# Performance work log

Hardware: AMD Instinct MI355X
Metric: run time of the kernel (lower is better)

## Reference

```python
import jax, jax.numpy as jnp
import numpy as np

B, C, H, W = 16, 256, 96, 96
PLANES = 64            # inplanes * ratio = 256 * 0.25
HEADS = 4
EPS = 1e-5             # BatchNorm eps


def setup_inputs() -> dict:
    key = jax.random.key(0)
    ks = jax.random.split(key, 8)
    HW = H * W
    G = HW // HEADS    # group size of the grouped 1x1 conv over spatial-positions-as-channels
    return {
        "x": jax.random.normal(ks[0], (B, C, H, W), jnp.float32),
        # input_conv: Conv1x1(C->PLANES) -> BN -> ReLU -> Conv1x1(PLANES->C)
        "w1": jax.random.normal(ks[1], (PLANES, C), jnp.float32) * (1.0 / np.sqrt(C)),
        "b1": jax.random.normal(ks[2], (PLANES,), jnp.float32) * 0.01,
        "gamma": jnp.ones((PLANES,), jnp.float32),
        "beta": jnp.zeros((PLANES,), jnp.float32),
        "mean": jnp.zeros((PLANES,), jnp.float32),
        "var": jnp.ones((PLANES,), jnp.float32),
        "w2": jax.random.normal(ks[3], (C, PLANES), jnp.float32) * (1.0 / np.sqrt(PLANES)),
        "b2": jax.random.normal(ks[4], (C,), jnp.float32) * 0.01,
        # conv_mask: Conv2d(HW, HEADS, k=1, groups=HEADS) -> weight [HEADS, G], bias [HEADS]
        "wm": jax.random.normal(ks[5], (HEADS, G), jnp.float32) * (1.0 / np.sqrt(G)),
        "bm": jax.random.normal(ks[6], (HEADS,), jnp.float32) * 0.01,
    }


def reference(x, w1, b1, gamma, beta, mean, var, w2, b2, wm, bm):
    Bx, Cx, Hx, Wx = x.shape
    G = (Hx * Wx) // HEADS
    # ---- input_conv: 1x1 conv -> BN (inference) -> ReLU -> 1x1 conv ----
    h = jnp.einsum('bchw,pc->bphw', x, w1) + b1[None, :, None, None]
    scale = (gamma / jnp.sqrt(var + EPS))[None, :, None, None]
    h = jax.nn.relu((h - mean[None, :, None, None]) * scale + beta[None, :, None, None])
    y = jnp.einsum('bphw,cp->bchw', h, w2) + b2[None, :, None, None]
    # ---- treat spatial positions as channels: [B, HEADS, G, C] ----
    ix = y.transpose(0, 2, 3, 1).reshape(Bx, HEADS, G, Cx)
    # grouped 1x1 conv over HW-channels -> logits [B, HEADS, C]
    logits = jnp.einsum('bhgc,hg->bhc', ix, wm) + bm[None, :, None]
    # softmax over channel axis (torch dim=2 of [B, HEADS, C, 1])
    mask = jax.nn.softmax(logits, axis=2)
    # context pooling matmul: [B,HEADS,G,C] @ [B,HEADS,C,1] -> [B,HEADS,G]
    ctx = jnp.einsum('bhgc,bhc->bhg', ix, mask)
    context = ctx.reshape(Bx, 1, Hx, Wx)
    # fusion_types = ('channel_add',)
    return x + context
```

## Files before the change

### kernel.cpp

```cpp
#include <hip/hip_runtime.h>

#define Bn 16
#define Cn 256
#define HWn 9216
#define Pn 64
#define HEADSn 4
#define Gn 2304
#define STILE 64
#define TILES_PER_B (HWn / STILE)
#define NTILE (Bn * TILES_PER_B)
#define CHUNK 9
#define NBLK (NTILE / CHUNK)

typedef float f32x4 __attribute__((ext_vector_type(4)));
typedef short short4v __attribute__((ext_vector_type(4)));
typedef short short8 __attribute__((ext_vector_type(8)));

static __device__ __forceinline__ unsigned short f2bf(float f) {
    unsigned int b = __builtin_bit_cast(unsigned int, f);
    unsigned int r = b + 0x7FFFu + ((b >> 16) & 1u);
    return (unsigned short)(r >> 16);
}
static __device__ __forceinline__ float bf2f(unsigned short u) {
    unsigned int b = ((unsigned int)u) << 16;
    return __builtin_bit_cast(float, b);
}
static __device__ __forceinline__ void gload_lds16(const void* g, void* l) {
    __builtin_amdgcn_global_load_lds((const __attribute__((address_space(1))) void*)g,
                                     (__attribute__((address_space(3))) void*)l, 16, 0, 0);
}

__global__ __launch_bounds__(256)
void k0_prep(const float* __restrict__ w1, const float* __restrict__ b1,
             const float* __restrict__ gamma, const float* __restrict__ beta,
             const float* __restrict__ mean, const float* __restrict__ var,
             float* __restrict__ bcv, short* __restrict__ w1b)
{
    const int gid = blockIdx.x * 256 + threadIdx.x;
    if (gid < 2048) {
        const int row = gid >> 5;
        const float s = gamma[row] * rsqrtf(var[row] + 1e-5f);
        const float* p = w1 + gid * 8;
        short8 v;
        #pragma unroll
        for (int j = 0; j < 8; ++j) v[j] = (short)f2bf(p[j] * s);
        *reinterpret_cast<short8*>(&w1b[gid * 8]) = v;
    }
    if (gid < Pn) {
        const float s = gamma[gid] * rsqrtf(var[gid] + 1e-5f);
        bcv[gid] = (b1[gid] - mean[gid]) * s + beta[gid];
    }
}

__global__ __launch_bounds__(256, 1)
void k1_gemm(const float* __restrict__ x, const short* __restrict__ w1b,
             const float* __restrict__ bcv, const float* __restrict__ wm,
             float* __restrict__ hmp, short* __restrict__ hg)
{
    __shared__ float xl[2][Cn * STILE];
    __shared__ float hml[4][Pn];

    const int pid  = blockIdx.x;
    const int b    = pid >> 4;
    const int t0b  = (pid & 15) * CHUNK;
    const int t    = threadIdx.x;
    const int lane = t & 63;
    const int wv   = t >> 6;
    const int wvu  = __builtin_amdgcn_readfirstlane(wv);
    const int g    = lane >> 4;
    const int m16  = lane & 15;
    const int sbase = wv * 16 + m16;

    short8 af[4][8];
    #pragma unroll
    for (int rt = 0; rt < 4; ++rt)
        #pragma unroll
        for (int ks = 0; ks < 8; ++ks)
            af[rt][ks] = *reinterpret_cast<const short8*>(
                w1b + (rt * 16 + m16) * Cn + ks * 32 + g * 8);

    float bc[4][4];
    #pragma unroll
    for (int rt = 0; rt < 4; ++rt)
        #pragma unroll
        for (int r = 0; r < 4; ++r) bc[rt][r] = bcv[rt * 16 + g * 4 + r];

    float hmacc[4][4];
    #pragma unroll
    for (int rt = 0; rt < 4; ++rt)
        #pragma unroll
        for (int r = 0; r < 4; ++r) hmacc[rt][r] = 0.f;

    const float* xbb = x + (size_t)b * Cn * HWn;

    #define STAGE(buf, tile)                                                     \
        do {                                                                     \
            const int _s0 = (tile) * STILE;                                      \
            _Pragma("unroll")                                                    \
            for (int i = 0; i < 16; ++i) {                                       \
                const int cbase = wvu * 64 + i * 4;                              \
                const int c     = cbase + g;                                     \
                const int gc    = (c >> 3) & 3;                                  \
                const int soff  = (m16 * 4) ^ (gc << 4);                         \
                gload_lds16(xbb + (size_t)c * HWn + _s0 + soff,                  \
                            &xl[buf][cbase * 64]);                               \
            }                                                                    \
        } while (0)

    STAGE(0, t0b);
    __syncthreads();

    int cur = 0;
    for (int it = 0; it < CHUNK; ++it) {
        if (it + 1 < CHUNK) STAGE(cur ^ 1, t0b + it + 1);

        const int s0 = (t0b + it) * STILE;
        const float* xc = xl[cur];
        const int srd = sbase ^ (g << 4);

        f32x4 acc[4] = { {0,0,0,0}, {0,0,0,0}, {0,0,0,0}, {0,0,0,0} };
        #pragma unroll
        for (int ks = 0; ks < 8; ++ks) {
            short8 bf;
            #pragma unroll
            for (int j = 0; j < 8; ++j) {
                const int k = ks * 32 + g * 8 + j;
                bf[j] = (short)f2bf(xc[k * 64 + srd]);
            }
            #pragma unroll
            for (int rt = 0; rt < 4; ++rt)
                acc[rt] = __builtin_amdgcn_mfma_f32_16x16x32_bf16(af[rt][ks], bf, acc[rt], 0, 0, 0);
        }

        const float wmv = wm[s0 + sbase];
        short* hrow = hg + ((size_t)b * HWn + s0 + sbase) * Pn;
        #pragma unroll
        for (int rt = 0; rt < 4; ++rt) {
            short4v hv;
            #pragma unroll
            for (int r = 0; r < 4; ++r) {
                float h = acc[rt][r] + bc[rt][r];
                h = h > 0.f ? h : 0.f;
                hmacc[rt][r] = fmaf(h, wmv, hmacc[rt][r]);
                hv[r] = (short)f2bf(h);
            }
            *reinterpret_cast<short4v*>(hrow + rt * 16 + g * 4) = hv;
        }

        __syncthreads();
        cur ^= 1;
    }

    #pragma unroll
    for (int rt = 0; rt < 4; ++rt)
        #pragma unroll
        for (int r = 0; r < 4; ++r) {
            float v = hmacc[rt][r];
            v += __shfl_xor(v, 1); v += __shfl_xor(v, 2);
            v += __shfl_xor(v, 4); v += __shfl_xor(v, 8);
            hmacc[rt][r] = v;
        }
    if (m16 == 0) {
        #pragma unroll
        for (int rt = 0; rt < 4; ++rt) {
            f32x4 hv = { hmacc[rt][0], hmacc[rt][1], hmacc[rt][2], hmacc[rt][3] };
            *reinterpret_cast<f32x4*>(&hml[wv][rt * 16 + g * 4]) = hv;
        }
    }
    __syncthreads();
    if (t < Pn) hmp[pid * Pn + t] = hml[0][t] + hml[1][t] + hml[2][t] + hml[3][t];
}

__global__ __launch_bounds__(256)
void k2_mask(const float* __restrict__ hmp, const float* __restrict__ w2,
             const float* __restrict__ b2, const float* __restrict__ wm,
             float* __restrict__ wmix, float* __restrict__ bmix)
{
    __shared__ float hms[Pn];
    __shared__ float masks[Cn];
    __shared__ float red[4];
    __shared__ float part[4][Pn];

    const int bh = blockIdx.x;
    const int head = bh & (HEADSn - 1);
    const int t = threadIdx.x;
    const int l = t & 63;
    const int wv = t >> 6;

    {
        const int p = t & 63, q = t >> 6;
        part[q][p] = hmp[(bh * 4 + q) * Pn + p];
    }
    __syncthreads();
    if (t < Pn) hms[t] = part[0][t] + part[1][t] + part[2][t] + part[3][t];
    __syncthreads();

    float wsum = 0.f;
    for (int i = t; i < Gn; i += 256) wsum += wm[head * Gn + i];
    #pragma unroll
    for (int d = 1; d < 64; d <<= 1) wsum += __shfl_xor(wsum, d);
    if (l == 0) red[wv] = wsum;
    __syncthreads();
    wsum = red[0] + red[1] + red[2] + red[3];

    float lg = 0.f;
    #pragma unroll
    for (int k = 0; k < Pn; ++k) lg = fmaf(w2[t * Pn + k], hms[k], lg);
    lg = fmaf(b2[t], wsum, lg);

    float mx = lg;
    #pragma unroll
    for (int d = 1; d < 64; d <<= 1) mx = fmaxf(mx, __shfl_xor(mx, d));
    __syncthreads();
    if (l == 0) red[wv] = mx;
    __syncthreads();
    mx = fmaxf(fmaxf(red[0], red[1]), fmaxf(red[2], red[3]));
    const float ev = __expf(lg - mx);
    float sm = ev;
    #pragma unroll
    for (int d = 1; d < 64; d <<= 1) sm += __shfl_xor(sm, d);
    __syncthreads();
    if (l == 0) red[wv] = sm;
    __syncthreads();
    sm = red[0] + red[1] + red[2] + red[3];
    masks[t] = ev / sm;
    __syncthreads();

    {
        const int k = t & (Pn - 1);
        const int q = t >> 6;
        float wp = 0.f;
        #pragma unroll
        for (int i = 0; i < 64; ++i) {
            const int c = q * 64 + i;
            wp = fmaf(masks[c], w2[c * Pn + k], wp);
        }
        part[q][k] = wp;
    }
    __syncthreads();
    if (t < Pn) wmix[bh * Pn + t] = part[0][t] + part[1][t] + part[2][t] + part[3][t];

    float bp = masks[t] * b2[t];
    #pragma unroll
    for (int d = 1; d < 64; d <<= 1) bp += __shfl_xor(bp, d);
    __syncthreads();
    if (l == 0) red[wv] = bp;
    __syncthreads();
    if (t == 0) bmix[bh] = red[0] + red[1] + red[2] + red[3];
}

__global__ __launch_bounds__(256)
void k3_stream(const float* __restrict__ x, const short* __restrict__ hg,
               const float* __restrict__ wmix, const float* __restrict__ bmix,
               float* __restrict__ out)
{
    __shared__ float ctxl[STILE];

    const int bid  = blockIdx.x;
    const int b    = bid / TILES_PER_B;
    const int tile = bid % TILES_PER_B;
    const int s0   = tile * STILE;
    const int head = s0 / Gn;
    const int bh   = b * HEADSn + head;
    const int t    = threadIdx.x;

    if (t < STILE) {
        const short* hr = hg + ((size_t)b * HWn + s0 + t) * Pn;
        const float* wmx = wmix + bh * Pn;
        float acc = 0.f;
        #pragma unroll
        for (int i = 0; i < 8; ++i) {
            const short8 v = *reinterpret_cast<const short8*>(hr + i * 8);
            const f32x4 w0 = *reinterpret_cast<const f32x4*>(wmx + i * 8);
            const f32x4 w1v = *reinterpret_cast<const f32x4*>(wmx + i * 8 + 4);
            #pragma unroll
            for (int j = 0; j < 4; ++j) {
                acc = fmaf(bf2f((unsigned short)v[j]), w0[j], acc);
                acc = fmaf(bf2f((unsigned short)v[4 + j]), w1v[j], acc);
            }
        }
        ctxl[t] = acc + bmix[bh];
    }
    __syncthreads();

    const int c0 = t >> 4;
    const int s4 = t & 15;
    const f32x4 cv = *reinterpret_cast<const f32x4*>(&ctxl[s4 * 4]);
    const float* xb = x + (size_t)b * Cn * HWn + s0 + s4 * 4;
    float* ob = out + (size_t)b * Cn * HWn + s0 + s4 * 4;
    #pragma unroll
    for (int i = 0; i < 16; ++i) {
        const size_t off = (size_t)(c0 + 16 * i) * HWn;
        *reinterpret_cast<f32x4*>(ob + off) =
            *reinterpret_cast<const f32x4*>(xb + off) + cv;
    }
}

extern "C" void kernel_launch(void* const* d_in, const int* in_sizes, int n_in,
                              void* d_out, int out_size, void* d_ws, size_t ws_size,
                              hipStream_t stream)
{
    (void)in_sizes; (void)n_in; (void)out_size; (void)ws_size;
    const float* x     = (const float*)d_in[0];
    const float* w1    = (const float*)d_in[1];
    const float* b1    = (const float*)d_in[2];
    const float* gamma = (const float*)d_in[3];
    const float* beta  = (const float*)d_in[4];
    const float* mean  = (const float*)d_in[5];
    const float* var   = (const float*)d_in[6];
    const float* w2    = (const float*)d_in[7];
    const float* b2    = (const float*)d_in[8];
    const float* wm    = (const float*)d_in[9];

    float* out  = (float*)d_out;
    float* wsf  = (float*)d_ws;
    float* hmp  = wsf;
    float* wmix = hmp + NBLK * Pn;
    float* bmix = wmix + Bn * HEADSn * Pn;
    float* bcv  = bmix + 64;
    short* w1b  = (short*)(bcv + 64);
    short* hg   = w1b + Pn * Cn;

    k0_prep<<<dim3(8), dim3(256), 0, stream>>>(w1, b1, gamma, beta, mean, var, bcv, w1b);
    k1_gemm<<<dim3(NBLK), dim3(256), 0, stream>>>(x, w1b, bcv, wm, hmp, hg);
    k2_mask<<<dim3(Bn * HEADSn), dim3(256), 0, stream>>>(hmp, w2, b2, wm, wmix, bmix);
    k3_stream<<<dim3(NTILE), dim3(256), 0, stream>>>(x, hg, wmix, bmix, out);
}
```

Baseline: 107.8 us.

## Split k1 GEMM into many small single-tile blocks with bf16 LDS staging

Replaces the persistent k1 kernel (256 blocks, each looping over 9 double-buffered 64-column tiles via global_load_lds) with 4608 small 128-thread blocks that each handle one 32-column tile. x is loaded with plain vector loads, converted to bf16 with v_cvt_pk_bf16_f32 and stored to a swizzled LDS layout, so LDS traffic and per-element conversions in the MFMA loop are reduced. Per-block hm partials go straight to global memory and k2 now sums 18 partials per head. This trades software pipelining for occupancy-based latency hiding, and adds more partial-sum traffic plus block launch overhead.

```diff
diff --git a/kernel.cpp b/kernel.cpp
--- a/kernel.cpp
+++ b/kernel.cpp
@@ -9,12 +9,13 @@
 #define STILE 64
 #define TILES_PER_B (HWn / STILE)
 #define NTILE (Bn * TILES_PER_B)
-#define CHUNK 9
-#define NBLK (NTILE / CHUNK)
+#define T32_PER_B 288
+#define NBLK1 (Bn * T32_PER_B)
 
 typedef float f32x4 __attribute__((ext_vector_type(4)));
 typedef short short4v __attribute__((ext_vector_type(4)));
 typedef short short8 __attribute__((ext_vector_type(8)));
+typedef unsigned int uint2v __attribute__((ext_vector_type(2)));
 
 static __device__ __forceinline__ unsigned short f2bf(float f) {
     unsigned int b = __builtin_bit_cast(unsigned int, f);
@@ -25,9 +26,10 @@
     unsigned int b = ((unsigned int)u) << 16;
     return __builtin_bit_cast(float, b);
 }
-static __device__ __forceinline__ void gload_lds16(const void* g, void* l) {
-    __builtin_amdgcn_global_load_lds((const __attribute__((address_space(1))) void*)g,
-                                     (__attribute__((address_space(3))) void*)l, 16, 0, 0);
+static __device__ __forceinline__ unsigned int cvtpk(float a, float b) {
+    unsigned int r;
+    asm("v_cvt_pk_bf16_f32 %0, %1, %2" : "=v"(r) : "v"(a), "v"(b));
+    return r;
 }
 
 __global__ __launch_bounds__(256)
@@ -52,107 +54,103 @@
     }
 }
 
-__global__ __launch_bounds__(256, 1)
+__global__ __launch_bounds__(128, 4)
 void k1_gemm(const float* __restrict__ x, const short* __restrict__ w1b,
              const float* __restrict__ bcv, const float* __restrict__ wm,
              float* __restrict__ hmp, short* __restrict__ hg)
 {
-    __shared__ float xl[2][Cn * STILE];
-    __shared__ float hml[4][Pn];
-
-    const int pid  = blockIdx.x;
-    const int b    = pid >> 4;
-    const int t0b  = (pid & 15) * CHUNK;
+    __shared__ short xl[Cn * 32];
+
+    const int bid  = blockIdx.x;
+    const int b    = bid / T32_PER_B;
+    const int t32  = bid % T32_PER_B;
+    const int s0   = t32 * 32;
     const int t    = threadIdx.x;
     const int lane = t & 63;
     const int wv   = t >> 6;
-    const int wvu  = __builtin_amdgcn_readfirstlane(wv);
     const int g    = lane >> 4;
     const int m16  = lane & 15;
-    const int sbase = wv * 16 + m16;
-
-    short8 af[4][8];
-    #pragma unroll
-    for (int rt = 0; rt < 4; ++rt)
+
+    short8 af[2][8];
+    #pragma unroll
+    for (int rt = 0; rt < 2; ++rt)
         #pragma unroll
         for (int ks = 0; ks < 8; ++ks)
             af[rt][ks] = *reinterpret_cast<const short8*>(
-                w1b + (rt * 16 + m16) * Cn + ks * 32 + g * 8);
-
-    float bc[4][4];
-    #pragma unroll
-    for (int rt = 0; rt < 4; ++rt)
-        #pragma unroll
-        for (int r = 0; r < 4; ++r) bc[rt][r] = bcv[rt * 16 + g * 4 + r];
-
-    float hmacc[4][4];
-    #pragma unroll
-    for (int rt = 0; rt < 4; ++rt)
-        #pragma unroll
-        for (int r = 0; r < 4; ++r) hmacc[rt][r] = 0.f;
-
-    const float* xbb = x + (size_t)b * Cn * HWn;
-
-    #define STAGE(buf, tile)                                                     \
-        do {                                                                     \
-            const int _s0 = (tile) * STILE;                                      \
-            _Pragma("unroll")                                                    \
-            for (int i = 0; i < 16; ++i) {                                       \
-                const int cbase = wvu * 64 + i * 4;                              \
-                const int c     = cbase + g;                                     \
-                const int gc    = (c >> 3) & 3;                                  \
-                const int soff  = (m16 * 4) ^ (gc << 4);                         \
-                gload_lds16(xbb + (size_t)c * HWn + _s0 + soff,                  \
-                            &xl[buf][cbase * 64]);                               \
-            }                                                                    \
-        } while (0)
-
-    STAGE(0, t0b);
-    __syncthreads();
-
-    int cur = 0;
-    for (int it = 0; it < CHUNK; ++it) {
-        if (it + 1 < CHUNK) STAGE(cur ^ 1, t0b + it + 1);
-
-        const int s0 = (t0b + it) * STILE;
-        const float* xc = xl[cur];
-        const int srd = sbase ^ (g << 4);
-
-        f32x4 acc[4] = { {0,0,0,0}, {0,0,0,0}, {0,0,0,0}, {0,0,0,0} };
-        #pragma unroll
-        for (int ks = 0; ks < 8; ++ks) {
+                w1b + (wv * 32 + rt * 16 + m16) * Cn + ks * 32 + g * 8);
+
+    float bc[2][4];
+    #pragma unroll
+    for (int rt = 0; rt < 2; ++rt)
+        #pragma unroll
+        for (int r = 0; r < 4; ++r) bc[rt][r] = bcv[wv * 32 + rt * 16 + g * 4 + r];
+
+    const int krow = t >> 3;
+    const int chk  = t & 7;
+    const float* xb = x + (size_t)b * Cn * HWn + s0 + chk * 4;
+    #pragma unroll
+    for (int i = 0; i < 16; ++i) {
+        const int k = i * 16 + krow;
+        const f32x4 v = *reinterpret_cast<const f32x4*>(xb + (size_t)k * HWn);
+        uint2v pk;
+        pk[0] = cvtpk(v[0], v[1]);
+        pk[1] = cvtpk(v[2], v[3]);
+        const int f    = (k ^ (k >> 2)) & 3;
+        const int byte = k * 64 + (((chk >> 1) ^ f) * 16) + (chk & 1) * 8;
+        *reinterpret_cast<uint2v*>(reinterpret_cast<char*>(xl) + byte) = pk;
+    }
+    __syncthreads();
+
+    f32x4 acc[2][2] = { { {0,0,0,0}, {0,0,0,0} }, { {0,0,0,0}, {0,0,0,0} } };
+    #pragma unroll
+    for (int ks = 0; ks < 8; ++ks) {
+        #pragma unroll
+        for (int cg = 0; cg < 2; ++cg) {
             short8 bf;
             #pragma unroll
             for (int j = 0; j < 8; ++j) {
-                const int k = ks * 32 + g * 8 + j;
-                bf[j] = (short)f2bf(xc[k * 64 + srd]);
+                const int k    = ks * 32 + g * 8 + j;
+                const int f    = (k ^ (k >> 2)) & 3;
+                const int byte = k * 64 + ((((cg * 2) + (m16 >> 3)) ^ f) * 16) + (m16 & 7) * 2;
+                bf[j] = *reinterpret_cast<const short*>(
+                    reinterpret_cast<const char*>(xl) + byte);
             }
-            #pragma unroll
-            for (int rt = 0; rt < 4; ++rt)
-                acc[rt] = __builtin_amdgcn_mfma_f32_16x16x32_bf16(af[rt][ks], bf, acc[rt], 0, 0, 0);
-        }
-
-        const float wmv = wm[s0 + sbase];
-        short* hrow = hg + ((size_t)b * HWn + s0 + sbase) * Pn;
-        #pragma unroll
-        for (int rt = 0; rt < 4; ++rt) {
-            short4v hv;
+            acc[cg][0] = __builtin_amdgcn_mfma_f32_16x16x32_bf16(af[0][ks], bf, acc[cg][0], 0, 0, 0);
+            acc[cg][1] = __builtin_amdgcn_mfma_f32_16x16x32_bf16(af[1][ks], bf, acc[cg][1], 0, 0, 0);
+        }
+    }
+
+    const float wmv0 = wm[s0 + m16];
+    const float wmv1 = wm[s0 + 16 + m16];
+    float hmacc[2][4];
+    #pragma unroll
+    for (int rt = 0; rt < 2; ++rt)
+        #pragma unroll
+        for (int r = 0; r < 4; ++r) hmacc[rt][r] = 0.f;
+
+    #pragma unroll
+    for (int cg = 0; cg < 2; ++cg) {
+        const float wmv = cg ? wmv1 : wmv0;
+        short* hrow = hg + ((size_t)b * HWn + s0 + cg * 16 + m16) * Pn + wv * 32;
+        #pragma unroll
+        for (int rt = 0; rt < 2; ++rt) {
+            float h[4];
             #pragma unroll
             for (int r = 0; r < 4; ++r) {
-                float h = acc[rt][r] + bc[rt][r];
-                h = h > 0.f ? h : 0.f;
-                hmacc[rt][r] = fmaf(h, wmv, hmacc[rt][r]);
-                hv[r] = (short)f2bf(h);
+                float hv = acc[cg][rt][r] + bc[rt][r];
+                hv = hv > 0.f ? hv : 0.f;
+                hmacc[rt][r] = fmaf(hv, wmv, hmacc[rt][r]);
+                h[r] = hv;
             }
-            *reinterpret_cast<short4v*>(hrow + rt * 16 + g * 4) = hv;
-        }
-
-        __syncthreads();
-        cur ^= 1;
-    }
-
-    #pragma unroll
-    for (int rt = 0; rt < 4; ++rt)
+            uint2v pk;
+            pk[0] = cvtpk(h[0], h[1]);
+            pk[1] = cvtpk(h[2], h[3]);
+            *reinterpret_cast<uint2v*>(hrow + rt * 16 + g * 4) = pk;
+        }
+    }
+
+    #pragma unroll
+    for (int rt = 0; rt < 2; ++rt)
         #pragma unroll
         for (int r = 0; r < 4; ++r) {
             float v = hmacc[rt][r];
@@ -162,13 +160,11 @@
         }
     if (m16 == 0) {
         #pragma unroll
-        for (int rt = 0; rt < 4; ++rt) {
-            f32x4 hv = { hmacc[rt][0], hmacc[rt][1], hmacc[rt][2], hmacc[rt][3] };
-            *reinterpret_cast<f32x4*>(&hml[wv][rt * 16 + g * 4]) = hv;
-        }
-    }
-    __syncthreads();
-    if (t < Pn) hmp[pid * Pn + t] = hml[0][t] + hml[1][t] + hml[2][t] + hml[3][t];
+        for (int rt = 0; rt < 2; ++rt)
+            #pragma unroll
+            for (int r = 0; r < 4; ++r)
+                hmp[bid * Pn + wv * 32 + rt * 16 + g * 4 + r] = hmacc[rt][r];
+    }
 }
 
 __global__ __launch_bounds__(256)
@@ -189,7 +185,11 @@
 
     {
         const int p = t & 63, q = t >> 6;
-        part[q][p] = hmp[(bh * 4 + q) * Pn + p];
+        const float* base = hmp + ((size_t)(bh >> 2) * T32_PER_B + head * 72) * Pn;
+        float sp = 0.f;
+        #pragma unroll
+        for (int jj = 0; jj < 18; ++jj) sp += base[(q + 4 * jj) * Pn + p];
+        part[q][p] = sp;
     }
     __syncthreads();
     if (t < Pn) hms[t] = part[0][t] + part[1][t] + part[2][t] + part[3][t];
@@ -315,14 +315,14 @@
     float* out  = (float*)d_out;
     float* wsf  = (float*)d_ws;
     float* hmp  = wsf;
-    float* wmix = hmp + NBLK * Pn;
+    float* wmix = hmp + NBLK1 * Pn;
     float* bmix = wmix + Bn * HEADSn * Pn;
     float* bcv  = bmix + 64;
     short* w1b  = (short*)(bcv + 64);
     short* hg   = w1b + Pn * Cn;
 
     k0_prep<<<dim3(8), dim3(256), 0, stream>>>(w1, b1, gamma, beta, mean, var, bcv, w1b);
-    k1_gemm<<<dim3(NBLK), dim3(256), 0, stream>>>(x, w1b, bcv, wm, hmp, hg);
+    k1_gemm<<<dim3(NBLK1), dim3(128), 0, stream>>>(x, w1b, bcv, wm, hmp, hg);
     k2_mask<<<dim3(Bn * HEADSn), dim3(256), 0, stream>>>(hmp, w2, b2, wm, wmix, bmix);
     k3_stream<<<dim3(NTILE), dim3(256), 0, stream>>>(x, hg, wmix, bmix, out);
 }
```

New measurement: 101.2 us. 6.1% less time.

## Restructure GEMM into many small-tile blocks and split context from streaming add

Applied to the files above, without the earlier changes.

The first GEMM kernel stops looping over nine double-buffered 64-column tiles per persistent block. It now launches one block per 128-column tile, stages channels in 64-row chunks, allows up to eight blocks per CU, and packs bf16 with v_cvt_pk_bf16_f32. The mask kernel sums over more per-tile partials. The per-position context dot product moves into its own kernel that writes a context buffer. The final add then streams whole channel rows with long contiguous vector accesses. This is meant to raise occupancy and memory-level parallelism and to make the large x read/out write more contiguous, at the cost of an extra launch, a context buffer round trip, and a non-overlapped load-then-compute GEMM loop.

```diff
diff --git a/kernel.cpp b/kernel.cpp
--- a/kernel.cpp
+++ b/kernel.cpp
@@ -6,15 +6,15 @@
 #define Pn 64
 #define HEADSn 4
 #define Gn 2304
-#define STILE 64
-#define TILES_PER_B (HWn / STILE)
-#define NTILE (Bn * TILES_PER_B)
-#define CHUNK 9
-#define NBLK (NTILE / CHUNK)
+#define ST1 128
+#define T1_PER_B (HWn / ST1)
+#define NBLK1 (Bn * T1_PER_B)
+#define TILES_PER_HEAD (Gn / ST1)
 
 typedef float f32x4 __attribute__((ext_vector_type(4)));
-typedef short short4v __attribute__((ext_vector_type(4)));
 typedef short short8 __attribute__((ext_vector_type(8)));
+typedef unsigned int uint2v __attribute__((ext_vector_type(2)));
+typedef unsigned int uint4v __attribute__((ext_vector_type(4)));
 
 static __device__ __forceinline__ unsigned short f2bf(float f) {
     unsigned int b = __builtin_bit_cast(unsigned int, f);
@@ -24,6 +24,11 @@
 static __device__ __forceinline__ float bf2f(unsigned short u) {
     unsigned int b = ((unsigned int)u) << 16;
     return __builtin_bit_cast(float, b);
+}
+static __device__ __forceinline__ unsigned int cvtpk(float a, float b) {
+    unsigned int r;
+    asm("v_cvt_pk_bf16_f32 %0, %1, %2" : "=v"(r) : "v"(a), "v"(b));
+    return r;
 }
 static __device__ __forceinline__ void gload_lds16(const void* g, void* l) {
     __builtin_amdgcn_global_load_lds((const __attribute__((address_space(1))) void*)g,
@@ -52,32 +57,33 @@
     }
 }
 
-__global__ __launch_bounds__(256, 1)
+__global__ __launch_bounds__(256, 8)
 void k1_gemm(const float* __restrict__ x, const short* __restrict__ w1b,
              const float* __restrict__ bcv, const float* __restrict__ wm,
              float* __restrict__ hmp, short* __restrict__ hg)
 {
-    __shared__ float xl[2][Cn * STILE];
+    __shared__ float xl[64 * ST1];
     __shared__ float hml[4][Pn];
 
     const int pid  = blockIdx.x;
-    const int b    = pid >> 4;
-    const int t0b  = (pid & 15) * CHUNK;
+    const int b    = pid / T1_PER_B;
+    const int st   = pid % T1_PER_B;
+    const int s0   = st * ST1;
     const int t    = threadIdx.x;
     const int lane = t & 63;
     const int wv   = t >> 6;
     const int wvu  = __builtin_amdgcn_readfirstlane(wv);
     const int g    = lane >> 4;
     const int m16  = lane & 15;
-    const int sbase = wv * 16 + m16;
+    const int scol0 = wv * 32 + m16;
 
     short8 af[4][8];
     #pragma unroll
     for (int rt = 0; rt < 4; ++rt)
         #pragma unroll
-        for (int ks = 0; ks < 8; ++ks)
-            af[rt][ks] = *reinterpret_cast<const short8*>(
-                w1b + (rt * 16 + m16) * Cn + ks * 32 + g * 8);
+        for (int kk = 0; kk < 8; ++kk)
+            af[rt][kk] = *reinterpret_cast<const short8*>(
+                w1b + (rt * 16 + m16) * Cn + kk * 32 + g * 8);
 
     float bc[4][4];
     #pragma unroll
@@ -85,70 +91,70 @@
         #pragma unroll
         for (int r = 0; r < 4; ++r) bc[rt][r] = bcv[rt * 16 + g * 4 + r];
 
+    const float* xbb = x + (size_t)b * Cn * HWn + s0;
+    f32x4 acc[2][4];
+    #pragma unroll
+    for (int cgi = 0; cgi < 2; ++cgi)
+        #pragma unroll
+        for (int rt = 0; rt < 4; ++rt) acc[cgi][rt] = f32x4{0.f, 0.f, 0.f, 0.f};
+
+    #pragma unroll
+    for (int kc = 0; kc < 4; ++kc) {
+        #pragma unroll
+        for (int i = 0; i < 8; ++i) {
+            const int c = kc * 64 + wvu * 16 + i * 2 + (lane >> 5);
+            gload_lds16(xbb + (size_t)c * HWn + (lane & 31) * 4,
+                        &xl[(wvu * 8 + i) * 256]);
+        }
+        __syncthreads();
+
+        #pragma unroll
+        for (int ks2 = 0; ks2 < 2; ++ks2) {
+            #pragma unroll
+            for (int cgi = 0; cgi < 2; ++cgi) {
+                const int sc = scol0 + cgi * 16;
+                uint4v bu;
+                #pragma unroll
+                for (int jp = 0; jp < 4; ++jp) {
+                    const int kl = ks2 * 32 + g * 8 + jp * 2;
+                    bu[jp] = cvtpk(xl[kl * ST1 + sc], xl[(kl + 1) * ST1 + sc]);
+                }
+                const short8 bf = __builtin_bit_cast(short8, bu);
+                #pragma unroll
+                for (int rt = 0; rt < 4; ++rt)
+                    acc[cgi][rt] = __builtin_amdgcn_mfma_f32_16x16x32_bf16(
+                        af[rt][kc * 2 + ks2], bf, acc[cgi][rt], 0, 0, 0);
+            }
+        }
+        __syncthreads();
+    }
+
     float hmacc[4][4];
     #pragma unroll
     for (int rt = 0; rt < 4; ++rt)
         #pragma unroll
         for (int r = 0; r < 4; ++r) hmacc[rt][r] = 0.f;
 
-    const float* xbb = x + (size_t)b * Cn * HWn;
-
-    #define STAGE(buf, tile)                                                     \
-        do {                                                                     \
-            const int _s0 = (tile) * STILE;                                      \
-            _Pragma("unroll")                                                    \
-            for (int i = 0; i < 16; ++i) {                                       \
-                const int cbase = wvu * 64 + i * 4;                              \
-                const int c     = cbase + g;                                     \
-                const int gc    = (c >> 3) & 3;                                  \
-                const int soff  = (m16 * 4) ^ (gc << 4);                         \
-                gload_lds16(xbb + (size_t)c * HWn + _s0 + soff,                  \
-                            &xl[buf][cbase * 64]);                               \
-            }                                                                    \
-        } while (0)
-
-    STAGE(0, t0b);
-    __syncthreads();
-
-    int cur = 0;
-    for (int it = 0; it < CHUNK; ++it) {
-        if (it + 1 < CHUNK) STAGE(cur ^ 1, t0b + it + 1);
-
-        const int s0 = (t0b + it) * STILE;
-        const float* xc = xl[cur];
-        const int srd = sbase ^ (g << 4);
-
-        f32x4 acc[4] = { {0,0,0,0}, {0,0,0,0}, {0,0,0,0}, {0,0,0,0} };
-        #pragma unroll
-        for (int ks = 0; ks < 8; ++ks) {
-            short8 bf;
-            #pragma unroll
-            for (int j = 0; j < 8; ++j) {
-                const int k = ks * 32 + g * 8 + j;
-                bf[j] = (short)f2bf(xc[k * 64 + srd]);
-            }
-            #pragma unroll
-            for (int rt = 0; rt < 4; ++rt)
-                acc[rt] = __builtin_amdgcn_mfma_f32_16x16x32_bf16(af[rt][ks], bf, acc[rt], 0, 0, 0);
-        }
-
-        const float wmv = wm[s0 + sbase];
-        short* hrow = hg + ((size_t)b * HWn + s0 + sbase) * Pn;
+    #pragma unroll
+    for (int cgi = 0; cgi < 2; ++cgi) {
+        const int sg = s0 + wv * 32 + cgi * 16 + m16;
+        const float wmv = wm[sg];
+        short* hrow = hg + ((size_t)b * HWn + sg) * Pn;
         #pragma unroll
         for (int rt = 0; rt < 4; ++rt) {
-            short4v hv;
+            float h[4];
             #pragma unroll
             for (int r = 0; r < 4; ++r) {
-                float h = acc[rt][r] + bc[rt][r];
-                h = h > 0.f ? h : 0.f;
-                hmacc[rt][r] = fmaf(h, wmv, hmacc[rt][r]);
-                hv[r] = (short)f2bf(h);
+                float hv = acc[cgi][rt][r] + bc[rt][r];
+                hv = hv > 0.f ? hv : 0.f;
+                hmacc[rt][r] = fmaf(hv, wmv, hmacc[rt][r]);
+                h[r] = hv;
             }
-            *reinterpret_cast<short4v*>(hrow + rt * 16 + g * 4) = hv;
-        }
-
-        __syncthreads();
-        cur ^= 1;
+            uint2v pk;
+            pk[0] = cvtpk(h[0], h[1]);
+            pk[1] = cvtpk(h[2], h[3]);
+            *reinterpret_cast<uint2v*>(hrow + rt * 16 + g * 4) = pk;
+        }
     }
 
     #pragma unroll
@@ -189,7 +195,14 @@
 
     {
         const int p = t & 63, q = t >> 6;
-        part[q][p] = hmp[(bh * 4 + q) * Pn + p];
+        const float* base = hmp + ((size_t)(bh >> 2) * T1_PER_B + head * TILES_PER_HEAD) * Pn;
+        float sp = 0.f;
+        #pragma unroll
+        for (int j = 0; j < 5; ++j) {
+            const int idx = q + 4 * j;
+            if (idx < TILES_PER_HEAD) sp += base[idx * Pn + p];
+        }
+        part[q][p] = sp;
     }
     __syncthreads();
     if (t < Pn) hms[t] = part[0][t] + part[1][t] + part[2][t] + part[3][t];
@@ -250,49 +263,59 @@
 }
 
 __global__ __launch_bounds__(256)
-void k3_stream(const float* __restrict__ x, const short* __restrict__ hg,
-               const float* __restrict__ wmix, const float* __restrict__ bmix,
+void k2b_ctx(const short* __restrict__ hg, const float* __restrict__ wmix,
+             const float* __restrict__ bmix, float* __restrict__ ctxb)
+{
+    const int bid = blockIdx.x;
+    const int b   = bid / 288;
+    const int s32 = bid % 288;
+    const int head = s32 / 72;
+    const int bh  = b * HEADSn + head;
+    const int t   = threadIdx.x;
+    const int sr  = t >> 3;
+    const int j8  = t & 7;
+    const int s   = s32 * 32 + sr;
+
+    const short8 hv = *reinterpret_cast<const short8*>(
+        hg + ((size_t)b * HWn + s) * Pn + j8 * 8);
+    const f32x4 w0 = *reinterpret_cast<const f32x4*>(wmix + bh * Pn + j8 * 8);
+    const f32x4 w1v = *reinterpret_cast<const f32x4*>(wmix + bh * Pn + j8 * 8 + 4);
+    float acc = 0.f;
+    #pragma unroll
+    for (int j = 0; j < 4; ++j) {
+        acc = fmaf(bf2f((unsigned short)hv[j]), w0[j], acc);
+        acc = fmaf(bf2f((unsigned short)hv[4 + j]), w1v[j], acc);
+    }
+    acc += __shfl_xor(acc, 1);
+    acc += __shfl_xor(acc, 2);
+    acc += __shfl_xor(acc, 4);
+    if (j8 == 0) ctxb[(size_t)b * HWn + s] = acc + bmix[bh];
+}
+
+__global__ __launch_bounds__(256)
+void k3_stream(const float* __restrict__ x, const float* __restrict__ ctxb,
                float* __restrict__ out)
 {
-    __shared__ float ctxl[STILE];
-
-    const int bid  = blockIdx.x;
-    const int b    = bid / TILES_PER_B;
-    const int tile = bid % TILES_PER_B;
-    const int s0   = tile * STILE;
-    const int head = s0 / Gn;
-    const int bh   = b * HEADSn + head;
-    const int t    = threadIdx.x;
-
-    if (t < STILE) {
-        const short* hr = hg + ((size_t)b * HWn + s0 + t) * Pn;
-        const float* wmx = wmix + bh * Pn;
-        float acc = 0.f;
-        #pragma unroll
-        for (int i = 0; i < 8; ++i) {
-            const short8 v = *reinterpret_cast<const short8*>(hr + i * 8);
-            const f32x4 w0 = *reinterpret_cast<const f32x4*>(wmx + i * 8);
-            const f32x4 w1v = *reinterpret_cast<const f32x4*>(wmx + i * 8 + 4);
-            #pragma unroll
-            for (int j = 0; j < 4; ++j) {
-                acc = fmaf(bf2f((unsigned short)v[j]), w0[j], acc);
-                acc = fmaf(bf2f((unsigned short)v[4 + j]), w1v[j], acc);
-            }
-        }
-        ctxl[t] = acc + bmix[bh];
-    }
-    __syncthreads();
-
-    const int c0 = t >> 4;
-    const int s4 = t & 15;
-    const f32x4 cv = *reinterpret_cast<const f32x4*>(&ctxl[s4 * 4]);
-    const float* xb = x + (size_t)b * Cn * HWn + s0 + s4 * 4;
-    float* ob = out + (size_t)b * Cn * HWn + s0 + s4 * 4;
-    #pragma unroll
-    for (int i = 0; i < 16; ++i) {
-        const size_t off = (size_t)(c0 + 16 * i) * HWn;
-        *reinterpret_cast<f32x4*>(ob + off) =
-            *reinterpret_cast<const f32x4*>(xb + off) + cv;
+    const int bid = blockIdx.x;
+    const int b   = bid >> 6;
+    const int c0  = (bid & 63) * 4;
+    const int t   = threadIdx.x;
+
+    f32x4 cv[9];
+    #pragma unroll
+    for (int j = 0; j < 9; ++j)
+        cv[j] = *reinterpret_cast<const f32x4*>(ctxb + (size_t)b * HWn + (j * 256 + t) * 4);
+
+    #pragma unroll
+    for (int ci = 0; ci < 4; ++ci) {
+        const float* xr = x + ((size_t)b * Cn + c0 + ci) * HWn;
+        float* orow = out + ((size_t)b * Cn + c0 + ci) * HWn;
+        #pragma unroll
+        for (int j = 0; j < 9; ++j) {
+            const int off = (j * 256 + t) * 4;
+            *reinterpret_cast<f32x4*>(orow + off) =
+                *reinterpret_cast<const f32x4*>(xr + off) + cv[j];
+        }
     }
 }
 
@@ -315,14 +338,16 @@
     float* out  = (float*)d_out;
     float* wsf  = (float*)d_ws;
     float* hmp  = wsf;
-    float* wmix = hmp + NBLK * Pn;
+    float* wmix = hmp + NBLK1 * Pn;
     float* bmix = wmix + Bn * HEADSn * Pn;
     float* bcv  = bmix + 64;
-    short* w1b  = (short*)(bcv + 64);
+    float* ctxb = bcv + 64;
+    short* w1b  = (short*)(ctxb + Bn * HWn);
     short* hg   = w1b + Pn * Cn;
 
     k0_prep<<<dim3(8), dim3(256), 0, stream>>>(w1, b1, gamma, beta, mean, var, bcv, w1b);
-    k1_gemm<<<dim3(NBLK), dim3(256), 0, stream>>>(x, w1b, bcv, wm, hmp, hg);
+    k1_gemm<<<dim3(NBLK1), dim3(256), 0, stream>>>(x, w1b, bcv, wm, hmp, hg);
     k2_mask<<<dim3(Bn * HEADSn), dim3(256), 0, stream>>>(hmp, w2, b2, wm, wmix, bmix);
-    k3_stream<<<dim3(NTILE), dim3(256), 0, stream>>>(x, hg, wmix, bmix, out);
-}
+    k2b_ctx<<<dim3(Bn * 288), dim3(256), 0, stream>>>(hg, wmix, bmix, ctxb);
+    k3_stream<<<dim3(Bn * 64), dim3(256), 0, stream>>>(x, ctxb, out);
+}
```

New measurement: 117.1 us. 1.09x slower.
